# Kernel optimization log

Hardware: AMD Instinct MI355X
Metric: run time of the kernel (lower is better)

## Reference

```python
import jax, jax.numpy as jnp
import numpy as np

NUM_HEADS = 16


def setup_inputs() -> dict:
    key = jax.random.key(0)
    k1, k2, k3 = jax.random.split(key, 3)
    B, S, D = 4, 2048, 1024
    hidden_states = jax.random.normal(k1, (B, S, D), dtype=jnp.float32)
    w_qkv = jax.random.normal(k2, (D, 3 * D), dtype=jnp.float32) * (1.0 / np.sqrt(D))
    w_out = jax.random.normal(k3, (D, D), dtype=jnp.float32) * (1.0 / np.sqrt(D))
    return {"hidden_states": hidden_states, "w_qkv": w_qkv, "w_out": w_out}


def reference(hidden_states, w_qkv, w_out):
    B, S, D = hidden_states.shape
    H = NUM_HEADS
    d = D // H
    # fused QKV projection: [B, S, 3D] -> [3, B, S, H, d]
    qkv = (hidden_states @ w_qkv).reshape(B, S, 3, H, d)
    q, k, v = jnp.moveaxis(qkv, 2, 0)  # each [B, S, H, d]
    scale = 1.0 / np.sqrt(d).astype(np.float32)
    scores = jnp.einsum("bqhd,bkhd->bhqk", q, k) * scale  # [B, H, S, S]
    attn = jax.nn.softmax(scores, axis=-1)
    ctx = jnp.einsum("bhqk,bkhd->bqhd", attn, v).reshape(B, S, D)
    return ctx @ w_out
```

## Files before the change

### kernel.cpp

```cpp
#include <hip/hip_runtime.h>
#include <hip/hip_bf16.h>
#include <math.h>

typedef __bf16 bf16;
typedef __bf16 bf16x4 __attribute__((ext_vector_type(4)));
typedef __bf16 bf16x8 __attribute__((ext_vector_type(8)));
typedef float  f32x4  __attribute__((ext_vector_type(4)));

#define B_  4
#define S_  2048
#define D_  1024
#define H_  16
#define DH  64
#define M_  (B_*S_)
#define BH_ (B_*H_)

#define QSCALE 0.18033688011112042f

__device__ __forceinline__ void glds16(const bf16* g, bf16* l) {
  __builtin_amdgcn_global_load_lds((const __attribute__((address_space(1))) void*)g,
                                   (__attribute__((address_space(3))) void*)l, 16, 0, 0);
}

__global__ __launch_bounds__(256) void prep(const float* __restrict__ hidden, bf16* __restrict__ hb,
                                            const float* __restrict__ wqkv, const float* __restrict__ wout,
                                            bf16* __restrict__ wqkvT, bf16* __restrict__ woutT) {
  int bx = blockIdx.x, tid = threadIdx.x;
  if (bx < 8192) {
    int i = (bx * 256 + tid) * 4;
    float4 v = *(const float4*)(hidden + i);
    bf16x4 o = { (bf16)v.x, (bf16)v.y, (bf16)v.z, (bf16)v.w };
    *(bf16x4*)(hb + i) = o;
    return;
  }
  __shared__ float tile[32][33];
  int t = bx - 8192;
  const float* in; bf16* out; int C, c0, r0;
  if (t < 96 * 32) { in = wqkv; out = wqkvT; C = 3072; c0 = (t % 96) * 32; r0 = (t / 96) * 32; }
  else { t -= 96 * 32;  in = wout; out = woutT; C = 1024; c0 = (t % 32) * 32; r0 = (t / 32) * 32; }
  int tx = tid & 31, ty = tid >> 5;
  #pragma unroll
  for (int i = ty; i < 32; i += 8) tile[i][tx] = in[(size_t)(r0 + i) * C + c0 + tx];
  __syncthreads();
  #pragma unroll
  for (int i = ty; i < 32; i += 8) out[(size_t)(c0 + i) * D_ + r0 + tx] = (bf16)tile[tx][i];
}

#define LDA2 32
#define SUB  (128 * LDA2)

__device__ __forceinline__ void gemm_core(const bf16* __restrict__ A, const bf16* __restrict__ Bt,
                                          int m0, int n0, bf16* As, bf16* Bs,
                                          int tid, f32x4 acc[4][4]) {
  int wave = tid >> 6, lane = tid & 63, quad = lane >> 4, l16 = lane & 15;
  int wm = (wave >> 1) * 64, wn = (wave & 1) * 64;
  int lr = lane >> 2, lc = (lane & 3) * 8;
  const bf16* gA = A  + (size_t)(m0 + wave * 32 + lr) * D_ + lc;
  const bf16* gB = Bt + (size_t)(n0 + wave * 32 + lr) * D_ + lc;
  bf16* lA = As + wave * 32 * LDA2;
  bf16* lB = Bs + wave * 32 * LDA2;
  for (int k0 = 0; k0 < D_; k0 += 64) {
    #pragma unroll
    for (int h = 0; h < 2; h++) {
      int kk = k0 + h * 32;
      glds16(gA + kk,           lA + h * SUB);
      glds16(gA + kk + 16 * D_, lA + h * SUB + 16 * LDA2);
      glds16(gB + kk,           lB + h * SUB);
      glds16(gB + kk + 16 * D_, lB + h * SUB + 16 * LDA2);
    }
    __syncthreads();
    #pragma unroll
    for (int h = 0; h < 2; h++) {
      bf16x8 af[4], bff[4];
      #pragma unroll
      for (int i = 0; i < 4; i++) af[i]  = *(const bf16x8*)(As + h * SUB + (wm + i * 16 + l16) * LDA2 + quad * 8);
      #pragma unroll
      for (int j = 0; j < 4; j++) bff[j] = *(const bf16x8*)(Bs + h * SUB + (wn + j * 16 + l16) * LDA2 + quad * 8);
      #pragma unroll
      for (int i = 0; i < 4; i++)
        #pragma unroll
        for (int j = 0; j < 4; j++)
          acc[i][j] = __builtin_amdgcn_mfma_f32_16x16x32_bf16(af[i], bff[j], acc[i][j], 0, 0, 0);
    }
    __syncthreads();
  }
}

__global__ __launch_bounds__(256) void gemm_qkv(const bf16* __restrict__ A, const bf16* __restrict__ Bt,
                                                bf16* __restrict__ Qb, bf16* __restrict__ Kb,
                                                bf16* __restrict__ Vtb) {
  __shared__ __attribute__((aligned(16))) bf16 As[2 * SUB];
  __shared__ __attribute__((aligned(16))) bf16 Bs[2 * SUB];
  int tid = threadIdx.x;
  int m0 = blockIdx.y * 128, n0 = blockIdx.x * 128;
  f32x4 acc[4][4] = {};
  gemm_core(A, Bt, m0, n0, As, Bs, tid, acc);
  int wave = tid >> 6, lane = tid & 63, quad = lane >> 4, l16 = lane & 15;
  int wm = (wave >> 1) * 64, wn = (wave & 1) * 64;
  int which = n0 >> 10;
  if (which == 2) {
    #pragma unroll
    for (int i = 0; i < 4; i++) {
      int mb = m0 + wm + i * 16 + quad * 4;
      int b = mb >> 11, s = mb & 2047;
      #pragma unroll
      for (int j = 0; j < 4; j++) {
        int n = n0 + wn + j * 16 + l16;
        int h = (n >> 6) & 15, dd = n & 63;
        bf16x4 v4 = { (bf16)acc[i][j][0], (bf16)acc[i][j][1], (bf16)acc[i][j][2], (bf16)acc[i][j][3] };
        *(bf16x4*)(Vtb + ((size_t)(b * H_ + h) * DH + dd) * S_ + s) = v4;
      }
    }
  } else {
    bf16* dst = (which == 0) ? Qb : Kb;
    float sc = (which == 0) ? QSCALE : 1.0f;
    #pragma unroll
    for (int i = 0; i < 4; i++) {
      #pragma unroll
      for (int j = 0; j < 4; j++) {
        int n = n0 + wn + j * 16 + l16;
        int h = (n >> 6) & 15, dd = n & 63;
        #pragma unroll
        for (int r = 0; r < 4; r++) {
          int m = m0 + wm + i * 16 + quad * 4 + r;
          int b = m >> 11, s = m & 2047;
          dst[(((size_t)(b * H_ + h)) * S_ + s) * DH + dd] = (bf16)(acc[i][j][r] * sc);
        }
      }
    }
  }
}

__global__ __launch_bounds__(256) void gemm_out(const bf16* __restrict__ A, const bf16* __restrict__ Bt,
                                                float* __restrict__ C) {
  __shared__ __attribute__((aligned(16))) bf16 As[2 * SUB];
  __shared__ __attribute__((aligned(16))) bf16 Bs[2 * SUB];
  int tid = threadIdx.x;
  int m0 = blockIdx.x * 128, n0 = blockIdx.y * 128;
  f32x4 acc[4][4] = {};
  gemm_core(A, Bt, m0, n0, As, Bs, tid, acc);
  int wave = tid >> 6, lane = tid & 63, quad = lane >> 4, l16 = lane & 15;
  int wm = (wave >> 1) * 64, wn = (wave & 1) * 64;
  #pragma unroll
  for (int i = 0; i < 4; i++)
    #pragma unroll
    for (int j = 0; j < 4; j++) {
      int n = n0 + wn + j * 16 + l16;
      #pragma unroll
      for (int r = 0; r < 4; r++) {
        int m = m0 + wm + i * 16 + quad * 4 + r;
        C[(size_t)m * D_ + n] = acc[i][j][r];
      }
    }
}

#define NT  (S_ / 64)

#define KVSW(row, col) (((row) * 64) + ((col) ^ (((row) & 7) << 3)))
#define PSW(row, col)  (((row) * 32) + ((col) ^ ((((row) >> 1) & 3) << 3)))

__global__ __launch_bounds__(256, 2) void attn(const bf16* __restrict__ Qb, const bf16* __restrict__ Kb,
                                               const bf16* __restrict__ Vtb, bf16* __restrict__ ctx) {
  __shared__ __attribute__((aligned(16))) bf16 Ks[2][64 * 64];
  __shared__ __attribute__((aligned(16))) bf16 Vs[2][64 * 64];
  __shared__ __attribute__((aligned(16))) bf16 Ps[4][64 * 32];
  int tid = threadIdx.x;
  int wave = tid >> 6, lane = tid & 63, quad = lane >> 4, l16 = lane & 15;
  int bh = blockIdx.x;
  int b = bh >> 4, h = bh & 15;
  int q0 = blockIdx.y * 256 + wave * 64;
  const bf16* Qp = Qb  + (size_t)bh * S_ * DH;
  const bf16* Kp = Kb  + (size_t)bh * S_ * DH;
  const bf16* Vp = Vtb + (size_t)bh * DH * S_;

  int srow = tid >> 3, scc = (tid & 7) << 3;
  int swz = KVSW(srow, scc);

  bf16x8 qf[4][2];
  #pragma unroll
  for (int nq = 0; nq < 4; nq++)
    #pragma unroll
    for (int ks = 0; ks < 2; ks++)
      qf[nq][ks] = *(const bf16x8*)(Qp + (size_t)(q0 + nq * 16 + l16) * DH + ks * 32 + quad * 8);

  bf16 one1 = (bf16)1.0f;
  bf16x8 onesf = { one1, one1, one1, one1, one1, one1, one1, one1 };

  f32x4 o[4][4] = {};
  f32x4 oden[4] = {};

  {
    bf16x8 k0a = *(const bf16x8*)(Kp + (size_t)srow * DH + scc);
    bf16x8 k0b = *(const bf16x8*)(Kp + (size_t)(32 + srow) * DH + scc);
    bf16x8 v0a = *(const bf16x8*)(Vp + (size_t)srow * S_ + scc);
    bf16x8 v0b = *(const bf16x8*)(Vp + (size_t)(32 + srow) * S_ + scc);
    *(bf16x8*)(Ks[0] + swz)             = k0a;
    *(bf16x8*)(Ks[0] + swz + 32 * 64)   = k0b;
    *(bf16x8*)(Vs[0] + swz)             = v0a;
    *(bf16x8*)(Vs[0] + swz + 32 * 64)   = v0b;
  }

  for (int kt = 0; kt < NT; kt++) {
    int cur = kt & 1;
    __syncthreads();

    bf16x8 ka, kb2, va, vb;
    if (kt + 1 < NT) {
      const bf16* Kn = Kp + (size_t)(kt + 1) * 64 * DH;
      const bf16* Vn = Vp + (size_t)(kt + 1) * 64;
      ka  = *(const bf16x8*)(Kn + (size_t)srow * DH + scc);
      kb2 = *(const bf16x8*)(Kn + (size_t)(32 + srow) * DH + scc);
      va  = *(const bf16x8*)(Vn + (size_t)srow * S_ + scc);
      vb  = *(const bf16x8*)(Vn + (size_t)(32 + srow) * S_ + scc);
    }

    bf16x8 vf[4][2];
    #pragma unroll
    for (int td = 0; td < 4; td++)
      #pragma unroll
      for (int ks = 0; ks < 2; ks++)
        vf[td][ks] = *(const bf16x8*)(Vs[cur] + KVSW(td * 16 + l16, ks * 32 + quad * 8));

    #pragma unroll
    for (int hh = 0; hh < 2; hh++) {
      #pragma unroll
      for (int kq2 = 0; kq2 < 2; kq2++) {
        int kq = hh * 2 + kq2;
        bf16x8 kfr[2];
        #pragma unroll
        for (int ks = 0; ks < 2; ks++)
          kfr[ks] = *(const bf16x8*)(Ks[cur] + KVSW(kq * 16 + l16, ks * 32 + quad * 8));
        #pragma unroll
        for (int nq = 0; nq < 4; nq++) {
          f32x4 st = {};
          __builtin_amdgcn_s_setprio(1);
          st = __builtin_amdgcn_mfma_f32_16x16x32_bf16(kfr[0], qf[nq][0], st, 0, 0, 0);
          st = __builtin_amdgcn_mfma_f32_16x16x32_bf16(kfr[1], qf[nq][1], st, 0, 0, 0);
          __builtin_amdgcn_s_setprio(0);
          bf16x4 pk;
          #pragma unroll
          for (int r = 0; r < 4; r++) pk[r] = (bf16)__builtin_amdgcn_exp2f(st[r]);
          *(bf16x4*)(&Ps[wave][PSW(nq * 16 + l16, kq2 * 16 + quad * 4)]) = pk;
        }
      }
      #pragma unroll
      for (int nq = 0; nq < 4; nq++) {
        bf16x8 pf = *(const bf16x8*)(&Ps[wave][PSW(nq * 16 + l16, quad * 8)]);
        __builtin_amdgcn_s_setprio(1);
        oden[nq] = __builtin_amdgcn_mfma_f32_16x16x32_bf16(pf, onesf, oden[nq], 0, 0, 0);
        #pragma unroll
        for (int td = 0; td < 4; td++)
          o[nq][td] = __builtin_amdgcn_mfma_f32_16x16x32_bf16(pf, vf[td][hh], o[nq][td], 0, 0, 0);
        __builtin_amdgcn_s_setprio(0);
      }
    }

    if (kt + 1 < NT) {
      int nxt = cur ^ 1;
      *(bf16x8*)(Ks[nxt] + swz)           = ka;
      *(bf16x8*)(Ks[nxt] + swz + 32 * 64) = kb2;
      *(bf16x8*)(Vs[nxt] + swz)           = va;
      *(bf16x8*)(Vs[nxt] + swz + 32 * 64) = vb;
    }
  }

  #pragma unroll
  for (int nq = 0; nq < 4; nq++) {
    #pragma unroll
    for (int r = 0; r < 4; r++) {
      float inv = 1.0f / oden[nq][r];
      int q = q0 + nq * 16 + quad * 4 + r;
      #pragma unroll
      for (int td = 0; td < 4; td++) {
        int dd = td * 16 + l16;
        ctx[((size_t)(b * S_) + q) * D_ + h * DH + dd] = (bf16)(o[nq][td][r] * inv);
      }
    }
  }
}

extern "C" void kernel_launch(void* const* d_in, const int* in_sizes, int n_in,
                              void* d_out, int out_size, void* d_ws, size_t ws_size,
                              hipStream_t stream) {
  (void)in_sizes; (void)n_in; (void)out_size; (void)ws_size;
  const float* hidden = (const float*)d_in[0];
  const float* w_qkv  = (const float*)d_in[1];
  const float* w_out  = (const float*)d_in[2];
  float* out = (float*)d_out;

  char* ws = (char*)d_ws;
  size_t off = 0;
  bf16* hb    = (bf16*)(ws + off); off += (size_t)M_ * D_ * 2;
  bf16* wqkvT = (bf16*)(ws + off); off += (size_t)3 * D_ * D_ * 2;
  bf16* woutT = (bf16*)(ws + off); off += (size_t)D_ * D_ * 2;
  bf16* Qb    = (bf16*)(ws + off); off += (size_t)M_ * D_ * 2;
  bf16* Kb    = (bf16*)(ws + off); off += (size_t)M_ * D_ * 2;
  bf16* Vtb   = (bf16*)(ws + off); off += (size_t)M_ * D_ * 2;
  bf16* ctxb  = hb;

  prep<<<8192 + 96 * 32 + 32 * 32, 256, 0, stream>>>(hidden, hb, w_qkv, w_out, wqkvT, woutT);
  gemm_qkv<<<dim3(3 * D_ / 128, M_ / 128), 256, 0, stream>>>(hb, wqkvT, Qb, Kb, Vtb);
  attn<<<dim3(BH_, S_ / 256), 256, 0, stream>>>(Qb, Kb, Vtb, ctxb);
  gemm_out<<<dim3(M_ / 128, D_ / 128), 256, 0, stream>>>(ctxb, woutT, out);
}
```

Measured before the change: 258.4 us.

## Use 256x128 triple-buffered swizzled GEMM pipeline and drop attention setprio

Replaces the 128x128 double-sync GEMM core with a 256x128, 512-thread block. It uses a three-stage direct-to-LDS load pipeline controlled by explicit vmcnt waits, and XOR-swizzled LDS rows to avoid bank conflicts. The goal is to overlap global loads with MFMA work and to raise operand reuse per block in both projection GEMMs. The cost is about 147KB of LDS and one block per CU, which leaves fewer blocks to hide latency. The attention kernel also stops raising wave priority around its MFMA calls.

New measurement: 255.9 us. No clear change (-1.0%).

```diff
diff --git a/kernel.cpp b/kernel.cpp
--- a/kernel.cpp
+++ b/kernel.cpp
@@ -46,55 +46,100 @@
   for (int i = ty; i < 32; i += 8) out[(size_t)(c0 + i) * D_ + r0 + tx] = (bf16)tile[tx][i];
 }
 
-#define LDA2 32
-#define SUB  (128 * LDA2)
-
-__device__ __forceinline__ void gemm_core(const bf16* __restrict__ A, const bf16* __restrict__ Bt,
-                                          int m0, int n0, bf16* As, bf16* Bs,
-                                          int tid, f32x4 acc[4][4]) {
-  int wave = tid >> 6, lane = tid & 63, quad = lane >> 4, l16 = lane & 15;
-  int wm = (wave >> 1) * 64, wn = (wave & 1) * 64;
-  int lr = lane >> 2, lc = (lane & 3) * 8;
-  const bf16* gA = A  + (size_t)(m0 + wave * 32 + lr) * D_ + lc;
-  const bf16* gB = Bt + (size_t)(n0 + wave * 32 + lr) * D_ + lc;
-  bf16* lA = As + wave * 32 * LDA2;
-  bf16* lB = Bs + wave * 32 * LDA2;
-  for (int k0 = 0; k0 < D_; k0 += 64) {
-    #pragma unroll
-    for (int h = 0; h < 2; h++) {
-      int kk = k0 + h * 32;
-      glds16(gA + kk,           lA + h * SUB);
-      glds16(gA + kk + 16 * D_, lA + h * SUB + 16 * LDA2);
-      glds16(gB + kk,           lB + h * SUB);
-      glds16(gB + kk + 16 * D_, lB + h * SUB + 16 * LDA2);
-    }
-    __syncthreads();
-    #pragma unroll
-    for (int h = 0; h < 2; h++) {
-      bf16x8 af[4], bff[4];
-      #pragma unroll
-      for (int i = 0; i < 4; i++) af[i]  = *(const bf16x8*)(As + h * SUB + (wm + i * 16 + l16) * LDA2 + quad * 8);
-      #pragma unroll
-      for (int j = 0; j < 4; j++) bff[j] = *(const bf16x8*)(Bs + h * SUB + (wn + j * 16 + l16) * LDA2 + quad * 8);
-      #pragma unroll
-      for (int i = 0; i < 4; i++)
-        #pragma unroll
-        for (int j = 0; j < 4; j++)
-          acc[i][j] = __builtin_amdgcn_mfma_f32_16x16x32_bf16(af[i], bff[j], acc[i][j], 0, 0, 0);
-    }
-    __syncthreads();
-  }
-}
-
-__global__ __launch_bounds__(256) void gemm_qkv(const bf16* __restrict__ A, const bf16* __restrict__ Bt,
-                                                bf16* __restrict__ Qb, bf16* __restrict__ Kb,
-                                                bf16* __restrict__ Vtb) {
-  __shared__ __attribute__((aligned(16))) bf16 As[2 * SUB];
-  __shared__ __attribute__((aligned(16))) bf16 Bs[2 * SUB];
+#define BM 256
+#define BN 128
+#define BK 64
+#define NTILE (D_ / BK)
+#define ATILE (BM * BK)
+#define BTILE (BN * BK)
+
+__device__ __forceinline__ void core256(const bf16* __restrict__ A, const bf16* __restrict__ Bt,
+                                        int m0, int n0, bf16* As, bf16* Bs, int tid,
+                                        f32x4 acc[4][4]) {
+  const int wave = tid >> 6, lane = tid & 63, quad = lane >> 4, l16 = lane & 15;
+  const int wm = (wave >> 1) * 64, wn = (wave & 1) * 64;
+  const int lr8 = lane >> 3, lg = lane & 7;
+  const int sg = ((lg ^ lr8) << 3);
+  const bf16* gA = A  + (size_t)(m0 + lr8) * D_ + sg;
+  const bf16* gB = Bt + (size_t)(n0 + lr8) * D_ + sg;
+  const int swq = ((quad ^ (l16 & 7)) << 3);
+  const int swq4 = (((4 + quad) ^ (l16 & 7)) << 3);
+
+#define STAGE256(slot, kt) do {                                                    \
+    int koff = (kt) * BK;                                                          \
+    bf16* a_d = As + (slot) * ATILE + wave * 2048;                                 \
+    bf16* b_d = Bs + (slot) * BTILE + wave * 1024;                                 \
+    _Pragma("unroll")                                                              \
+    for (int i_ = 0; i_ < 4; i_++)                                                 \
+      glds16(gA + (size_t)(wave * 32 + i_ * 8) * D_ + koff, a_d + i_ * 512);       \
+    _Pragma("unroll")                                                              \
+    for (int i_ = 0; i_ < 2; i_++)                                                 \
+      glds16(gB + (size_t)(wave * 16 + i_ * 8) * D_ + koff, b_d + i_ * 512);       \
+  } while (0)
+
+#define KSTEP256(slot) do {                                                        \
+    const bf16* a_s = As + (slot) * ATILE;                                         \
+    const bf16* b_s = Bs + (slot) * BTILE;                                         \
+    bf16x8 af[2][4], bfr[2][4];                                                    \
+    _Pragma("unroll")                                                              \
+    for (int i_ = 0; i_ < 4; i_++) {                                               \
+      af[0][i_] = *(const bf16x8*)(a_s + (wm + i_ * 16 + l16) * 64 + swq);         \
+      af[1][i_] = *(const bf16x8*)(a_s + (wm + i_ * 16 + l16) * 64 + swq4);        \
+    }                                                                              \
+    _Pragma("unroll")                                                              \
+    for (int j_ = 0; j_ < 4; j_++) {                                               \
+      bfr[0][j_] = *(const bf16x8*)(b_s + (wn + j_ * 16 + l16) * 64 + swq);        \
+      bfr[1][j_] = *(const bf16x8*)(b_s + (wn + j_ * 16 + l16) * 64 + swq4);       \
+    }                                                                              \
+    _Pragma("unroll")                                                              \
+    for (int kk_ = 0; kk_ < 2; kk_++)                                              \
+      _Pragma("unroll")                                                            \
+      for (int i_ = 0; i_ < 4; i_++)                                               \
+        _Pragma("unroll")                                                          \
+        for (int j_ = 0; j_ < 4; j_++)                                             \
+          acc[i_][j_] = __builtin_amdgcn_mfma_f32_16x16x32_bf16(af[kk_][i_], bfr[kk_][j_], acc[i_][j_], 0, 0, 0); \
+  } while (0)
+
+  STAGE256(0, 0); STAGE256(1, 1); STAGE256(2, 2);
+  int sl = 0;
+  for (int t = 0; t <= NTILE - 4; t++) {
+    asm volatile("s_waitcnt vmcnt(12)" ::: "memory");
+    __builtin_amdgcn_sched_barrier(0);
+    __builtin_amdgcn_s_barrier();
+    __builtin_amdgcn_sched_barrier(0);
+    KSTEP256(sl);
+    __builtin_amdgcn_s_barrier();
+    __builtin_amdgcn_sched_barrier(0);
+    STAGE256(sl, t + 3);
+    sl = (sl == 2) ? 0 : sl + 1;
+  }
+  asm volatile("s_waitcnt vmcnt(12)" ::: "memory");
+  __builtin_amdgcn_sched_barrier(0);
+  __builtin_amdgcn_s_barrier(); __builtin_amdgcn_sched_barrier(0);
+  KSTEP256(sl); sl = (sl == 2) ? 0 : sl + 1;
+  __builtin_amdgcn_s_barrier(); __builtin_amdgcn_sched_barrier(0);
+  asm volatile("s_waitcnt vmcnt(6)" ::: "memory");
+  __builtin_amdgcn_sched_barrier(0);
+  __builtin_amdgcn_s_barrier(); __builtin_amdgcn_sched_barrier(0);
+  KSTEP256(sl); sl = (sl == 2) ? 0 : sl + 1;
+  __builtin_amdgcn_s_barrier(); __builtin_amdgcn_sched_barrier(0);
+  asm volatile("s_waitcnt vmcnt(0)" ::: "memory");
+  __builtin_amdgcn_sched_barrier(0);
+  __builtin_amdgcn_s_barrier(); __builtin_amdgcn_sched_barrier(0);
+  KSTEP256(sl);
+#undef STAGE256
+#undef KSTEP256
+}
+
+__global__ __launch_bounds__(512, 1) void gemm_qkv(const bf16* __restrict__ A, const bf16* __restrict__ Bt,
+                                                   bf16* __restrict__ Qb, bf16* __restrict__ Kb,
+                                                   bf16* __restrict__ Vtb) {
+  __shared__ __attribute__((aligned(16))) bf16 As[3 * ATILE];
+  __shared__ __attribute__((aligned(16))) bf16 Bs[3 * BTILE];
   int tid = threadIdx.x;
-  int m0 = blockIdx.y * 128, n0 = blockIdx.x * 128;
+  int m0 = blockIdx.y * BM, n0 = blockIdx.x * BN;
   f32x4 acc[4][4] = {};
-  gemm_core(A, Bt, m0, n0, As, Bs, tid, acc);
+  core256(A, Bt, m0, n0, As, Bs, tid, acc);
   int wave = tid >> 6, lane = tid & 63, quad = lane >> 4, l16 = lane & 15;
   int wm = (wave >> 1) * 64, wn = (wave & 1) * 64;
   int which = n0 >> 10;
@@ -131,14 +176,14 @@
   }
 }
 
-__global__ __launch_bounds__(256) void gemm_out(const bf16* __restrict__ A, const bf16* __restrict__ Bt,
-                                                float* __restrict__ C) {
-  __shared__ __attribute__((aligned(16))) bf16 As[2 * SUB];
-  __shared__ __attribute__((aligned(16))) bf16 Bs[2 * SUB];
+__global__ __launch_bounds__(512, 1) void gemm_out(const bf16* __restrict__ A, const bf16* __restrict__ Bt,
+                                                   float* __restrict__ C) {
+  __shared__ __attribute__((aligned(16))) bf16 As[3 * ATILE];
+  __shared__ __attribute__((aligned(16))) bf16 Bs[3 * BTILE];
   int tid = threadIdx.x;
-  int m0 = blockIdx.x * 128, n0 = blockIdx.y * 128;
+  int m0 = blockIdx.x * BM, n0 = blockIdx.y * BN;
   f32x4 acc[4][4] = {};
-  gemm_core(A, Bt, m0, n0, As, Bs, tid, acc);
+  core256(A, Bt, m0, n0, As, Bs, tid, acc);
   int wave = tid >> 6, lane = tid & 63, quad = lane >> 4, l16 = lane & 15;
   int wm = (wave >> 1) * 64, wn = (wave & 1) * 64;
   #pragma unroll
@@ -233,10 +278,8 @@
         #pragma unroll
         for (int nq = 0; nq < 4; nq++) {
           f32x4 st = {};
-          __builtin_amdgcn_s_setprio(1);
           st = __builtin_amdgcn_mfma_f32_16x16x32_bf16(kfr[0], qf[nq][0], st, 0, 0, 0);
           st = __builtin_amdgcn_mfma_f32_16x16x32_bf16(kfr[1], qf[nq][1], st, 0, 0, 0);
-          __builtin_amdgcn_s_setprio(0);
           bf16x4 pk;
           #pragma unroll
           for (int r = 0; r < 4; r++) pk[r] = (bf16)__builtin_amdgcn_exp2f(st[r]);
@@ -246,12 +289,10 @@
       #pragma unroll
       for (int nq = 0; nq < 4; nq++) {
         bf16x8 pf = *(const bf16x8*)(&Ps[wave][PSW(nq * 16 + l16, quad * 8)]);
-        __builtin_amdgcn_s_setprio(1);
         oden[nq] = __builtin_amdgcn_mfma_f32_16x16x32_bf16(pf, onesf, oden[nq], 0, 0, 0);
         #pragma unroll
         for (int td = 0; td < 4; td++)
           o[nq][td] = __builtin_amdgcn_mfma_f32_16x16x32_bf16(pf, vf[td][hh], o[nq][td], 0, 0, 0);
-        __builtin_amdgcn_s_setprio(0);
       }
     }
 
@@ -299,7 +340,7 @@
   bf16* ctxb  = hb;
 
   prep<<<8192 + 96 * 32 + 32 * 32, 256, 0, stream>>>(hidden, hb, w_qkv, w_out, wqkvT, woutT);
-  gemm_qkv<<<dim3(3 * D_ / 128, M_ / 128), 256, 0, stream>>>(hb, wqkvT, Qb, Kb, Vtb);
+  gemm_qkv<<<dim3(3 * D_ / BN, M_ / BM), 512, 0, stream>>>(hb, wqkvT, Qb, Kb, Vtb);
   attn<<<dim3(BH_, S_ / 256), 256, 0, stream>>>(Qb, Kb, Vtb, ctxb);
-  gemm_out<<<dim3(M_ / 128, D_ / 128), 256, 0, stream>>>(ctxb, woutT, out);
-}
+  gemm_out<<<dim3(M_ / BM, D_ / BN), 512, 0, stream>>>(ctxb, woutT, out);
+}
```
